# Kernel tuning notes

Measured on AMD Instinct MI355X. Metric: run time of the kernel, lower is better.

Reference implementation:

```python
import jax, jax.numpy as jnp
import numpy as np

K_MASK = -2.3819763e+38

B, T, D = 2, 2048, 2048
N_HEADS, N_KV, HEAD_DIM = 16, 8, 128
SCALAR = 0.08838834764831845  # head_dim ** -0.5
ROPE_BASE = 10000


def rms_norm(x, scale):
    # fp32 mean-of-squares, rsqrt, bf16 round-trip, then scale (as in QwemmaRMSNorm)
    x32 = x.astype(jnp.float32)
    var = jnp.mean(jnp.square(x32), axis=-1, keepdims=True)
    rescaled = (x32 * jax.lax.rsqrt(var + 1e-06)).astype(jnp.bfloat16)
    return rescaled * scale


def apply_rope(inputs, positions, base_frequency):
    head_dim = inputs.shape[-1]
    fraction = 2 * jnp.arange(0, head_dim // 2) / head_dim
    timescale = base_frequency ** fraction
    sinusoid = positions[..., jnp.newaxis] / timescale[jnp.newaxis, jnp.newaxis, :]
    sinusoid = sinusoid[..., jnp.newaxis, :]  # [B,T,1,H/2]
    sin = jnp.sin(sinusoid).astype(inputs.dtype)
    cos = jnp.cos(sinusoid).astype(inputs.dtype)
    first, second = jnp.split(inputs, 2, axis=-1)
    out = jnp.concatenate([first * cos - second * sin,
                           second * cos + first * sin], axis=-1)
    return out.astype(inputs.dtype)


def setup_inputs() -> dict:
    key = jax.random.key(0)
    ks = jax.random.split(key, 7)
    x = jax.random.normal(ks[0], (B, T, D), dtype=jnp.float32)
    segment_pos = jnp.broadcast_to(jnp.arange(T, dtype=jnp.int32)[None, :], (B, T))
    attn_mask = jnp.broadcast_to(jnp.tril(jnp.ones((T, T), dtype=bool))[None], (B, T, T))
    q_w = jax.random.normal(ks[1], (N_HEADS, D, HEAD_DIM), dtype=jnp.float32) * 0.02
    kv_w = jax.random.normal(ks[2], (2, N_KV, D, HEAD_DIM), dtype=jnp.float32) * 0.02
    o_w = jax.random.normal(ks[3], (N_HEADS, HEAD_DIM, D), dtype=jnp.float32) * 0.02
    q_scale = 1.0 + 0.1 * jax.random.normal(ks[4], (HEAD_DIM,), dtype=jnp.float32)
    k_scale = 1.0 + 0.1 * jax.random.normal(ks[5], (HEAD_DIM,), dtype=jnp.float32)
    return {"x": x, "segment_pos": segment_pos, "attn_mask": attn_mask,
            "q_w": q_w, "kv_w": kv_w, "o_w": o_w,
            "q_scale": q_scale, "k_scale": k_scale}


def reference(x, segment_pos, attn_mask, q_w, kv_w, o_w, q_scale, k_scale):
    # projections
    q = jnp.einsum('BTD,NDH->BTNH', x, q_w)
    k, v = jnp.einsum('BSD,CKDH->CBSKH', x, kv_w)
    # QK RMSNorm + RoPE
    q = apply_rope(rms_norm(q, q_scale), segment_pos, ROPE_BASE)
    k = apply_rope(rms_norm(k, k_scale), segment_pos, ROPE_BASE)
    # GQA: [B,T,N,H] -> [B,T,K,G,H]
    b, t, n, h = q.shape
    g = n // N_KV
    q = q.reshape((b, t, N_KV, g, h))
    logits = jnp.einsum('BTKGH,BSKH->BTKGS', q, k)
    logits = (logits.astype(jnp.float32) * SCALAR).astype(jnp.bfloat16)
    s = logits.shape[-1]
    logits = logits.reshape((b, t, n, s))
    padded = jnp.where(jnp.expand_dims(attn_mask, -2), logits, K_MASK)
    probs = jax.nn.softmax(padded.astype(jnp.float32), axis=-1).astype(k.dtype)
    probs = probs.reshape((b, t, N_KV, g, s))
    encoded = jnp.einsum('BTKGS,BSKH->BTKGH', probs, v)
    encoded = encoded.reshape((b, t, n, h))
    return jnp.einsum('BTNH,NHD->BTD', encoded, o_w)


if __name__ == '__main__':
    out = reference(**setup_inputs())
    print(out.shape, out.dtype)
```

## Files before the change

kernel.cpp:

```cpp
#include <hip/hip_runtime.h>

typedef unsigned short u16;
typedef __attribute__((ext_vector_type(4))) float f32x4;
typedef __attribute__((ext_vector_type(8))) short s16x8;

#define SCALAR_F 0.08838834764831845f
#define KMASKF (-1e30f)

__device__ __forceinline__ u16 f2b(float f){
  unsigned u = __float_as_uint(f);
  unsigned r = u + 0x7FFFu + ((u>>16)&1u);
  return (u16)(r>>16);
}
__device__ __forceinline__ float b2f(u16 h){ return __uint_as_float(((unsigned)h)<<16); }

__device__ __forceinline__ f32x4 mfma16(s16x8 a, s16x8 b, f32x4 c){
  return __builtin_amdgcn_mfma_f32_16x16x32_bf16(a, b, c, 0, 0, 0);
}

__device__ __forceinline__ void glds16(const u16* g, u16* l){
  __builtin_amdgcn_global_load_lds((const __attribute__((address_space(1))) unsigned*)g,
                                   (__attribute__((address_space(3))) unsigned*)l, 16, 0, 0);
}

#define PHASE_BAR() asm volatile("s_barrier" ::: "memory")
#define LGKM0()     do { asm volatile("s_waitcnt lgkmcnt(0)" ::: "memory"); __builtin_amdgcn_sched_barrier(0); } while(0)

__global__ __launch_bounds__(256) void cvt_f32_bf16(const float* __restrict__ in, u16* __restrict__ out){
  int i = blockIdx.x*256 + threadIdx.x;
  const float4* p = (const float4*)in;
  float4 a = p[2*i], b = p[2*i+1];
  s16x8 r;
  r[0]=(short)f2b(a.x); r[1]=(short)f2b(a.y); r[2]=(short)f2b(a.z); r[3]=(short)f2b(a.w);
  r[4]=(short)f2b(b.x); r[5]=(short)f2b(b.y); r[6]=(short)f2b(b.z); r[7]=(short)f2b(b.w);
  *(s16x8*)(out + (size_t)i*8) = r;
}

__global__ __launch_bounds__(256) void build_wqkvt(const float* __restrict__ qw, const float* __restrict__ kvw,
                                                   u16* __restrict__ out){
  __shared__ float t[64][65];
  int head = blockIdx.z;
  int d0 = blockIdx.y*64, h0 = blockIdx.x*64;
  const float* src; int colbase;
  if (head < 16){ src = qw + (size_t)head*2048*128; colbase = head*128; }
  else if (head < 24){ int k = head-16; src = kvw + (size_t)k*2048*128; colbase = 2048 + k*128; }
  else { int k = head-24; src = kvw + (size_t)(8+k)*2048*128; colbase = 3072 + k*128; }
  int tid = threadIdx.x;
  #pragma unroll
  for (int p=0;p<16;p++){ int e = p*256+tid; int r = e>>6, c = e&63;
    t[r][c] = src[(size_t)(d0+r)*128 + h0 + c]; }
  __syncthreads();
  #pragma unroll
  for (int p=0;p<16;p++){ int e = p*256+tid; int c = e>>6, r = e&63;
    out[(size_t)(colbase + h0 + c)*2048 + d0 + r] = f2b(t[r][c]); }
}

__global__ __launch_bounds__(256) void tr2048(const float* __restrict__ src, u16* __restrict__ out){
  __shared__ float t[64][65];
  int r0 = blockIdx.y*64, c0 = blockIdx.x*64;
  int tid = threadIdx.x;
  #pragma unroll
  for (int p=0;p<16;p++){ int e = p*256+tid; int r = e>>6, c = e&63;
    t[r][c] = src[(size_t)(r0+r)*2048 + c0 + c]; }
  __syncthreads();
  #pragma unroll
  for (int p=0;p<16;p++){ int e = p*256+tid; int c = e>>6, r = e&63;
    out[(size_t)(c0+c)*2048 + r0 + r] = f2b(t[r][c]); }
}

__global__ __launch_bounds__(256) void rope_table(float* __restrict__ table){
  int tid = blockIdx.x*256 + threadIdx.x;
  int pos = tid>>6, i = tid&63;
  float ts = powf(10000.f, (float)i * (1.f/64.f));
  float ang = (float)pos / ts;
  ((float2*)table)[tid] = make_float2(sinf(ang), cosf(ang));
}

__global__ __launch_bounds__(512,2) void gemm256(const u16* __restrict__ A, const u16* __restrict__ Bt,
                                                 u16* __restrict__ C, int K, int ldc){
  __shared__ u16 Als[2][2][128*64];
  __shared__ u16 Bls[2][2][128*64];
  const int tid = threadIdx.x;
  const int wid = tid>>6, l = tid&63;
  const int wr = wid>>2, wc = wid&3;
  const int l15 = l&15, lg = l>>4;
  const int wg = blockIdx.x;
  const int swz = (wg&7)*32 + (wg>>3);
  const size_t m0 = (size_t)(swz>>4)*256, n0 = (size_t)(swz&15)*256;

  const f32x4 z4 = {0.f,0.f,0.f,0.f};
  f32x4 acc[8][4];
  #pragma unroll
  for (int mi=0;mi<8;mi++)
    #pragma unroll
    for (int ni=0;ni<4;ni++) acc[mi][ni] = z4;

  auto stageA = [&](int k0, int bi, int h){
    #pragma unroll
    for (int c=0;c<2;c++){
      int g = c*512 + tid;
      int row = g>>3, pg = g&7;
      glds16(A + (m0 + h*128 + row)*K + k0 + ((pg ^ (row&7))<<3), &Als[bi][h][0] + g*8);
    }
  };
  auto stageB = [&](int k0, int bi, int h){
    #pragma unroll
    for (int c=0;c<2;c++){
      int g = c*512 + tid;
      int row = g>>3, pg = g&7;
      glds16(Bt + (n0 + h*128 + row)*K + k0 + ((pg ^ (row&7))<<3), &Bls[bi][h][0] + g*8);
    }
  };

  s16x8 af[8][2], bf[4][2];

  const int NT = K>>6;
  stageA(0,0,0); stageA(0,0,1); stageB(0,0,0); stageB(0,0,1);
  stageA(64,1,0); stageA(64,1,1);
  asm volatile("s_waitcnt vmcnt(4)" ::: "memory");
  PHASE_BAR();

  for (int t=0; t<NT; ++t){
    const int bi = t&1;
    const char* Ab = (const char*)&Als[bi][wr][0];
    const char* Bb = (const char*)&Bls[bi][wc>>1][0];
    const int brl = (wc&1)*64;
    const int kn1 = (t+1)<<6, kn2 = (t+2)<<6;

    #pragma unroll
    for (int mi=0;mi<4;mi++){
      int r = mi*16 + l15;
      #pragma unroll
      for (int kk=0;kk<2;kk++)
        af[mi][kk] = *(const s16x8*)(Ab + r*128 + (((kk*4+lg) ^ (r&7))<<4));
    }
    #pragma unroll
    for (int ni=0;ni<2;ni++){
      int r = brl + ni*16 + l15;
      #pragma unroll
      for (int kk=0;kk<2;kk++)
        bf[ni][kk] = *(const s16x8*)(Bb + r*128 + (((kk*4+lg) ^ (r&7))<<4));
    }
    if (t+1 < NT) stageB(kn1, bi^1, 0);
    PHASE_BAR(); LGKM0();
    __builtin_amdgcn_s_setprio(1);
    #pragma unroll
    for (int mi=0;mi<4;mi++)
      #pragma unroll
      for (int ni=0;ni<2;ni++)
        #pragma unroll
        for (int kk=0;kk<2;kk++)
          acc[mi][ni] = mfma16(af[mi][kk], bf[ni][kk], acc[mi][ni]);
    __builtin_amdgcn_s_setprio(0);
    PHASE_BAR();

    #pragma unroll
    for (int ni=2;ni<4;ni++){
      int r = brl + ni*16 + l15;
      #pragma unroll
      for (int kk=0;kk<2;kk++)
        bf[ni][kk] = *(const s16x8*)(Bb + r*128 + (((kk*4+lg) ^ (r&7))<<4));
    }
    if (t+1 < NT) stageB(kn1, bi^1, 1);
    PHASE_BAR(); LGKM0();
    __builtin_amdgcn_s_setprio(1);
    #pragma unroll
    for (int mi=0;mi<4;mi++)
      #pragma unroll
      for (int ni=2;ni<4;ni++)
        #pragma unroll
        for (int kk=0;kk<2;kk++)
          acc[mi][ni] = mfma16(af[mi][kk], bf[ni][kk], acc[mi][ni]);
    __builtin_amdgcn_s_setprio(0);
    PHASE_BAR();

    #pragma unroll
    for (int mi=4;mi<8;mi++){
      int r = mi*16 + l15;
      #pragma unroll
      for (int kk=0;kk<2;kk++)
        af[mi][kk] = *(const s16x8*)(Ab + r*128 + (((kk*4+lg) ^ (r&7))<<4));
    }
    PHASE_BAR(); LGKM0();
    __builtin_amdgcn_s_setprio(1);
    #pragma unroll
    for (int mi=4;mi<8;mi++)
      #pragma unroll
      for (int ni=2;ni<4;ni++)
        #pragma unroll
        for (int kk=0;kk<2;kk++)
          acc[mi][ni] = mfma16(af[mi][kk], bf[ni][kk], acc[mi][ni]);
    __builtin_amdgcn_s_setprio(0);
    PHASE_BAR();

    if (t+2 < NT){ stageA(kn2, bi, 0); stageA(kn2, bi, 1); }
    __builtin_amdgcn_s_setprio(1);
    #pragma unroll
    for (int mi=4;mi<8;mi++)
      #pragma unroll
      for (int ni=0;ni<2;ni++)
        #pragma unroll
        for (int kk=0;kk<2;kk++)
          acc[mi][ni] = mfma16(af[mi][kk], bf[ni][kk], acc[mi][ni]);
    __builtin_amdgcn_s_setprio(0);
    if (t < NT-2)      { asm volatile("s_waitcnt vmcnt(4)" ::: "memory"); }
    else if (t == NT-2){ asm volatile("s_waitcnt vmcnt(0)" ::: "memory"); }
    PHASE_BAR();
  }

  #pragma unroll
  for (int mi=0;mi<8;mi++)
    #pragma unroll
    for (int ni=0;ni<4;ni++)
      #pragma unroll
      for (int r=0;r<4;r++){
        size_t row = m0 + wr*128 + mi*16 + lg*4 + r;
        size_t col = n0 + wc*64 + ni*16 + l15;
        C[row*ldc + col] = f2b(acc[mi][ni][r]);
      }
}

__global__ __launch_bounds__(512,1) void gemm_o(const u16* __restrict__ A, const u16* __restrict__ Bt,
                                                float* __restrict__ C, int K, int ldc){
  __shared__ u16 Als[2][2][128*64];
  __shared__ u16 Bls[2][128*64];
  const int tid = threadIdx.x;
  const int wid = tid>>6, l = tid&63;
  const int wr = wid>>1, wc = wid&1;
  const int l15 = l&15, lg = l>>4;
  const int wg = blockIdx.x;
  const int swz = (wg&7)*32 + (wg>>3);
  const size_t m0 = (size_t)(swz>>4)*256, n0 = (size_t)(swz&15)*128;

  const f32x4 z4 = {0.f,0.f,0.f,0.f};
  f32x4 acc[4][4];
  #pragma unroll
  for (int mi=0;mi<4;mi++)
    #pragma unroll
    for (int ni=0;ni<4;ni++) acc[mi][ni] = z4;

  auto stageA = [&](int k0, int bi, int h){
    #pragma unroll
    for (int c=0;c<2;c++){
      int g = c*512 + tid;
      int row = g>>3, pg = g&7;
      glds16(A + (m0 + h*128 + row)*K + k0 + ((pg ^ (row&7))<<3), &Als[bi][h][0] + g*8);
    }
  };
  auto stageB = [&](int k0, int bi){
    #pragma unroll
    for (int c=0;c<2;c++){
      int g = c*512 + tid;
      int row = g>>3, pg = g&7;
      glds16(Bt + (n0 + row)*K + k0 + ((pg ^ (row&7))<<3), &Bls[bi][0] + g*8);
    }
  };

  s16x8 af[4][2], bf[4][2];

  const int NT = K>>6;
  stageA(0,0,0); stageA(0,0,1); stageB(0,0);
  stageA(64,1,0); stageA(64,1,1);
  asm volatile("s_waitcnt vmcnt(4)" ::: "memory");
  PHASE_BAR();

  for (int t=0; t<NT; ++t){
    const int bi = t&1;
    const char* Ab = (const char*)&Als[bi][wr>>1][0];
    const char* Bb = (const char*)&Bls[bi][0];
    const int arl = (wr&1)*64;
    const int brl = wc*64;
    const int kn1 = (t+1)<<6, kn2 = (t+2)<<6;

    #pragma unroll
    for (int mi=0;mi<2;mi++){
      int r = arl + mi*16 + l15;
      #pragma unroll
      for (int kk=0;kk<2;kk++)
        af[mi][kk] = *(const s16x8*)(Ab + r*128 + (((kk*4+lg) ^ (r&7))<<4));
    }
    #pragma unroll
    for (int ni=0;ni<2;ni++){
      int r = brl + ni*16 + l15;
      #pragma unroll
      for (int kk=0;kk<2;kk++)
        bf[ni][kk] = *(const s16x8*)(Bb + r*128 + (((kk*4+lg) ^ (r&7))<<4));
    }
    if (t+1 < NT) stageB(kn1, bi^1);
    PHASE_BAR(); LGKM0();
    __builtin_amdgcn_s_setprio(1);
    #pragma unroll
    for (int mi=0;mi<2;mi++)
      #pragma unroll
      for (int ni=0;ni<2;ni++)
        #pragma unroll
        for (int kk=0;kk<2;kk++)
          acc[mi][ni] = mfma16(af[mi][kk], bf[ni][kk], acc[mi][ni]);
    __builtin_amdgcn_s_setprio(0);
    PHASE_BAR();

    #pragma unroll
    for (int mi=2;mi<4;mi++){
      int r = arl + mi*16 + l15;
      #pragma unroll
      for (int kk=0;kk<2;kk++)
        af[mi][kk] = *(const s16x8*)(Ab + r*128 + (((kk*4+lg) ^ (r&7))<<4));
    }
    #pragma unroll
    for (int ni=2;ni<4;ni++){
      int r = brl + ni*16 + l15;
      #pragma unroll
      for (int kk=0;kk<2;kk++)
        bf[ni][kk] = *(const s16x8*)(Bb + r*128 + (((kk*4+lg) ^ (r&7))<<4));
    }
    PHASE_BAR(); LGKM0();
    __builtin_amdgcn_s_setprio(1);
    #pragma unroll
    for (int mi=0;mi<2;mi++)
      #pragma unroll
      for (int ni=2;ni<4;ni++)
        #pragma unroll
        for (int kk=0;kk<2;kk++)
          acc[mi][ni] = mfma16(af[mi][kk], bf[ni][kk], acc[mi][ni]);
    __builtin_amdgcn_s_setprio(0);
    PHASE_BAR();

    if (t+2 < NT){ stageA(kn2, bi, 0); stageA(kn2, bi, 1); }
    __builtin_amdgcn_s_setprio(1);
    #pragma unroll
    for (int mi=2;mi<4;mi++)
      #pragma unroll
      for (int ni=0;ni<4;ni++)
        #pragma unroll
        for (int kk=0;kk<2;kk++)
          acc[mi][ni] = mfma16(af[mi][kk], bf[ni][kk], acc[mi][ni]);
    __builtin_amdgcn_s_setprio(0);
    if (t < NT-2)      { asm volatile("s_waitcnt vmcnt(4)" ::: "memory"); }
    else if (t == NT-2){ asm volatile("s_waitcnt vmcnt(0)" ::: "memory"); }
    PHASE_BAR();
  }

  #pragma unroll
  for (int mi=0;mi<4;mi++)
    #pragma unroll
    for (int ni=0;ni<4;ni++)
      #pragma unroll
      for (int r=0;r<4;r++){
        size_t row = m0 + wr*64 + mi*16 + lg*4 + r;
        size_t col = n0 + wc*64 + ni*16 + l15;
        C[row*ldc + col] = acc[mi][ni][r];
      }
}

__global__ __launch_bounds__(256) void norm_rope(const u16* __restrict__ qkv, const float* __restrict__ table,
                                                 const float* __restrict__ scale, const int* __restrict__ segpos,
                                                 u16* __restrict__ dst, int nhl2, int colbase, float mult){
  int w = threadIdx.x>>6, l = threadIdx.x&63;
  int rid = blockIdx.x*4 + w;
  int bt = rid >> nhl2;
  int n  = rid & ((1<<nhl2)-1);
  int b = bt >> 11, t = bt & 2047;
  const u16* src = qkv + (size_t)bt*4096 + colbase + n*128;
  float x1 = b2f(src[l]), x2 = b2f(src[64+l]);
  float ss = x1*x1 + x2*x2;
  #pragma unroll
  for (int off=32; off; off>>=1) ss += __shfl_xor(ss, off);
  float rs = rsqrtf(ss*(1.f/128.f) + 1e-6f);
  float v1 = x1*rs*scale[l], v2 = x2*rs*scale[64+l];
  int pos = segpos[bt];
  float2 sc = ((const float2*)table)[pos*64 + l];
  float o1 = (v1*sc.y - v2*sc.x)*mult;
  float o2 = (v2*sc.y + v1*sc.x)*mult;
  u16* d = dst + (((size_t)((b<<nhl2) + n))*2048 + t)*128;
  d[l] = f2b(o1); d[64+l] = f2b(o2);
}

__global__ __launch_bounds__(256) void vtr(const u16* __restrict__ qkv, u16* __restrict__ vt){
  __shared__ float t[64][65];
  int bk = blockIdx.z;
  int t0 = blockIdx.y*64, d0 = blockIdx.x*64;
  int b = bk>>3, kv = bk&7;
  int tid = threadIdx.x;
  #pragma unroll
  for (int p=0;p<16;p++){ int e = p*256+tid; int r = e>>6, c = e&63;
    t[r][c] = b2f(qkv[(size_t)(b*2048 + t0 + r)*4096 + 3072 + kv*128 + d0 + c]); }
  __syncthreads();
  #pragma unroll
  for (int p=0;p<16;p++){ int e = p*256+tid; int c = e>>6, r = e&63;
    vt[((size_t)bk*128 + d0 + c)*2048 + t0 + r] = f2b(t[r][c]); }
}

__global__ __launch_bounds__(256,2) void attn_kern(const u16* __restrict__ qn, const u16* __restrict__ kn,
                                                   const u16* __restrict__ vt, u16* __restrict__ enc){
  __shared__ u16 Ks[2][64*128];
  __shared__ u16 Vs[2][64*128];
  __shared__ u16 Ps[4*16*64];
  const int idx = blockIdx.x;
  const int pp = idx>>5;
  const int hb = idx & 31;
  const int hn = hb & 15, b = hb >> 4;
  const int kv = hn>>1;
  const int tid = threadIdx.x, w = tid>>6, l = tid&63;
  const int l15 = l&15, lg = l>>4;
  const u16* qh = qn + ((size_t)(b*16+hn))*2048*128;
  const u16* kh = kn + ((size_t)(b*8+kv))*2048*128;
  const u16* vh = vt + ((size_t)(b*8+kv))*128*2048;
  const int qbA = pp, qbB = 31-pp;

  int qr0 = qbA*64 + w*16;
  s16x8 qf[4];
  #pragma unroll
  for (int kb=0;kb<4;kb++)
    qf[kb] = *(const s16x8*)(qh + (size_t)(qr0 + l15)*128 + kb*32 + lg*8);

  const f32x4 z4 = {0.f,0.f,0.f,0.f};
  f32x4 o[8];
  #pragma unroll
  for (int dn=0;dn<8;dn++) o[dn] = z4;
  float mrow[4], lp[4];
  #pragma unroll
  for (int r=0;r<4;r++){ mrow[r] = KMASKF; lp[r] = 0.f; }

  const char* KsB0 = (const char*)&Ks[0][0];
  const char* VsB0 = (const char*)&Vs[0][0];
  char* PsB = (char*)Ps + w*2048;

  auto stage = [&](int s0, int bi){
    #pragma unroll
    for (int i=0;i<4;i++){
      int slot = (w*4+i)*64 + l;
      { int row = slot>>4, g = slot&15, gl = g ^ (row&7);
        glds16(kh + (size_t)(s0+row)*128 + gl*8, &Ks[bi][0] + slot*8); }
      { int row = slot>>3, g = slot&7, gl = g ^ (row&7);
        glds16(vh + (size_t)row*2048 + s0 + gl*8, &Vs[bi][0] + slot*8); }
    }
  };

  auto epilogue = [&](int qr){
    #pragma unroll
    for (int r=0;r<4;r++){
      float s = lp[r];
      s += __shfl_xor(s,1); s += __shfl_xor(s,2); s += __shfl_xor(s,4); s += __shfl_xor(s,8);
      lp[r] = 1.f/s;
    }
    #pragma unroll
    for (int dn=0;dn<8;dn++)
      #pragma unroll
      for (int r=0;r<4;r++){
        size_t row = (size_t)b*2048 + qr + lg*4 + r;
        size_t col = hn*128 + dn*16 + l15;
        enc[row*2048 + col] = f2b(o[dn][r]*lp[r]);
      }
  };

  stage(0, 0);
  __syncthreads();

  int cur = 0;
  for (int it=0; it<=32; ++it){
    if (it < 32){
      int s0n = (it+1 <= pp) ? (it+1)*64 : (it-pp)*64;
      stage(s0n, cur^1);
    }
    const int s0 = (it <= pp) ? it*64 : (it-pp-1)*64;
    const char* KsB = KsB0 + cur*16384;
    const char* VsB = VsB0 + cur*16384;

    f32x4 sa[4];
    #pragma unroll
    for (int nc=0;nc<4;nc++) sa[nc] = z4;
    #pragma unroll
    for (int kb=0;kb<4;kb++){
      s16x8 kf[4];
      #pragma unroll
      for (int nc=0;nc<4;nc++){
        int srow = nc*16 + l15;
        int cb = (kb*64 + lg*16) ^ ((srow&7)<<4);
        kf[nc] = *(const s16x8*)(KsB + srow*256 + cb);
      }
      __builtin_amdgcn_s_setprio(1);
      #pragma unroll
      for (int nc=0;nc<4;nc++)
        sa[nc] = mfma16(qf[kb], kf[nc], sa[nc]);
      __builtin_amdgcn_s_setprio(0);
    }
    if (it == pp || it == 32){
      #pragma unroll
      for (int nc=0;nc<4;nc++)
        #pragma unroll
        for (int r=0;r<4;r++){
          int row = qr0 + lg*4 + r;
          int col = s0 + nc*16 + l15;
          if (col > row) sa[nc][r] = KMASKF;
        }
    }
    #pragma unroll
    for (int r=0;r<4;r++){
      float pm = fmaxf(fmaxf(sa[0][r], sa[1][r]), fmaxf(sa[2][r], sa[3][r]));
      pm = fmaxf(pm, __shfl_xor(pm,1));
      pm = fmaxf(pm, __shfl_xor(pm,2));
      pm = fmaxf(pm, __shfl_xor(pm,4));
      pm = fmaxf(pm, __shfl_xor(pm,8));
      float mo = mrow[r];
      float mn = mo;
      if (!__all(pm <= mo + 8.f)){
        mn = fmaxf(mo, pm);
        float sc = __expf(mo - mn);
        mrow[r] = mn;
        lp[r] *= sc;
        #pragma unroll
        for (int dn=0;dn<8;dn++) o[dn][r] *= sc;
      }
      int rowp = lg*4 + r;
      float ls = 0.f;
      #pragma unroll
      for (int nc=0;nc<4;nc++){
        float p = __expf(sa[nc][r] - mn);
        ls += p;
        int cb = ((nc*16 + l15)*2) ^ ((rowp&7)<<4);
        *(u16*)(PsB + rowp*128 + cb) = f2b(p);
      }
      lp[r] += ls;
    }
    asm volatile("" ::: "memory");
    #pragma unroll
    for (int kb=0;kb<2;kb++){
      int rowp = l15;
      int cbp = (kb*64 + lg*16) ^ ((rowp&7)<<4);
      s16x8 pf = *(const s16x8*)(PsB + rowp*128 + cbp);
      #pragma unroll
      for (int dn=0;dn<8;dn++){
        int vrow = dn*16 + l15;
        int cb = (kb*64 + lg*16) ^ ((vrow&7)<<4);
        s16x8 vf = *(const s16x8*)(VsB + vrow*128 + cb);
        __builtin_amdgcn_s_setprio(1);
        o[dn] = mfma16(pf, vf, o[dn]);
        __builtin_amdgcn_s_setprio(0);
      }
    }
    if (it == pp){
      epilogue(qr0);
      qr0 = qbB*64 + w*16;
      #pragma unroll
      for (int kb=0;kb<4;kb++)
        qf[kb] = *(const s16x8*)(qh + (size_t)(qr0 + l15)*128 + kb*32 + lg*8);
      #pragma unroll
      for (int dn=0;dn<8;dn++) o[dn] = z4;
      #pragma unroll
      for (int r=0;r<4;r++){ mrow[r] = KMASKF; lp[r] = 0.f; }
    }
    __syncthreads();
    cur ^= 1;
  }
  epilogue(qr0);
}

extern "C" void kernel_launch(void* const* d_in, const int* in_sizes, int n_in,
                              void* d_out, int out_size, void* d_ws, size_t ws_size,
                              hipStream_t stream){
  const float* x      = (const float*)d_in[0];
  const int*   segpos = (const int*)d_in[1];
  const float* qw     = (const float*)d_in[3];
  const float* kvw    = (const float*)d_in[4];
  const float* ow     = (const float*)d_in[5];
  const float* qs     = (const float*)d_in[6];
  const float* ks     = (const float*)d_in[7];
  float* out = (float*)d_out;

  char* ws = (char*)d_ws;
  size_t off = 0;
  auto alloc = [&](size_t bytes)->void*{ void* p = ws + off; off += (bytes + 255) & ~(size_t)255; return p; };
  u16*   xb    = (u16*)alloc((size_t)4096*2048*2);
  u16*   wqkvt = (u16*)alloc((size_t)4096*2048*2);
  u16*   wot   = (u16*)alloc((size_t)2048*2048*2);
  u16*   qkv   = (u16*)alloc((size_t)4096*4096*2);
  u16*   qn    = (u16*)alloc((size_t)2*16*2048*128*2);
  u16*   kn    = (u16*)alloc((size_t)2*8*2048*128*2);
  u16*   vt    = (u16*)alloc((size_t)2*8*128*2048*2);
  u16*   enc   = (u16*)alloc((size_t)4096*2048*2);
  float* table = (float*)alloc((size_t)2048*64*2*4);

  cvt_f32_bf16<<<4096,256,0,stream>>>(x, xb);
  build_wqkvt<<<dim3(2,32,32),256,0,stream>>>(qw, kvw, wqkvt);
  tr2048<<<dim3(32,32),256,0,stream>>>(ow, wot);
  rope_table<<<512,256,0,stream>>>(table);
  gemm256<<<256,512,0,stream>>>(xb, wqkvt, qkv, 2048, 4096);
  norm_rope<<<16384,256,0,stream>>>(qkv, table, qs, segpos, qn, 4, 0,    SCALAR_F);
  norm_rope<<<8192, 256,0,stream>>>(qkv, table, ks, segpos, kn, 3, 2048, 1.0f);
  vtr<<<dim3(2,32,16),256,0,stream>>>(qkv, vt);
  attn_kern<<<512,256,0,stream>>>(qn, kn, vt, enc);
  gemm_o<<<256,512,0,stream>>>(enc, wot, out, 2048, 2048);
}
```

Baseline: 366.2 us.

## Merge prep and norm kernels, drop lazy rescale and setprio in attention

Merges the x conversion and rope-table kernels into one launch, the two weight-transpose kernels into another, and the Q and K norm_rope launches into one grid, cutting the launch count from ten to seven. Each merged kernel picks its work by block index. In the attention inner loop, the conditional lazy rescale (skip unless the max grows by more than 8) becomes an unconditional rescale of the accumulators on every tile. The s_setprio hints around the MFMA calls are also removed. The unconditional rescale adds per-tile multiplies but removes a wave-wide vote and branch.

Result: faster. 354.0 us (-3.3%).

```diff
diff --git a/kernel.cpp b/kernel.cpp
--- a/kernel.cpp
+++ b/kernel.cpp
@@ -26,54 +26,57 @@
 #define PHASE_BAR() asm volatile("s_barrier" ::: "memory")
 #define LGKM0()     do { asm volatile("s_waitcnt lgkmcnt(0)" ::: "memory"); __builtin_amdgcn_sched_barrier(0); } while(0)
 
-__global__ __launch_bounds__(256) void cvt_f32_bf16(const float* __restrict__ in, u16* __restrict__ out){
-  int i = blockIdx.x*256 + threadIdx.x;
-  const float4* p = (const float4*)in;
-  float4 a = p[2*i], b = p[2*i+1];
-  s16x8 r;
-  r[0]=(short)f2b(a.x); r[1]=(short)f2b(a.y); r[2]=(short)f2b(a.z); r[3]=(short)f2b(a.w);
-  r[4]=(short)f2b(b.x); r[5]=(short)f2b(b.y); r[6]=(short)f2b(b.z); r[7]=(short)f2b(b.w);
-  *(s16x8*)(out + (size_t)i*8) = r;
-}
-
-__global__ __launch_bounds__(256) void build_wqkvt(const float* __restrict__ qw, const float* __restrict__ kvw,
-                                                   u16* __restrict__ out){
+__global__ __launch_bounds__(256) void prep_misc(const float* __restrict__ in, u16* __restrict__ out,
+                                                 float* __restrict__ table){
+  int bid = blockIdx.x;
+  if (bid < 4096){
+    int i = bid*256 + threadIdx.x;
+    const float4* p = (const float4*)in;
+    float4 a = p[2*i], b = p[2*i+1];
+    s16x8 r;
+    r[0]=(short)f2b(a.x); r[1]=(short)f2b(a.y); r[2]=(short)f2b(a.z); r[3]=(short)f2b(a.w);
+    r[4]=(short)f2b(b.x); r[5]=(short)f2b(b.y); r[6]=(short)f2b(b.z); r[7]=(short)f2b(b.w);
+    *(s16x8*)(out + (size_t)i*8) = r;
+  } else {
+    int tid = (bid-4096)*256 + threadIdx.x;
+    int pos = tid>>6, i = tid&63;
+    float ts = powf(10000.f, (float)i * (1.f/64.f));
+    float ang = (float)pos / ts;
+    ((float2*)table)[tid] = make_float2(sinf(ang), cosf(ang));
+  }
+}
+
+__global__ __launch_bounds__(256) void prep_w(const float* __restrict__ qw, const float* __restrict__ kvw,
+                                              const float* __restrict__ ow,
+                                              u16* __restrict__ wqkvt, u16* __restrict__ wot){
   __shared__ float t[64][65];
-  int head = blockIdx.z;
-  int d0 = blockIdx.y*64, h0 = blockIdx.x*64;
-  const float* src; int colbase;
-  if (head < 16){ src = qw + (size_t)head*2048*128; colbase = head*128; }
-  else if (head < 24){ int k = head-16; src = kvw + (size_t)k*2048*128; colbase = 2048 + k*128; }
-  else { int k = head-24; src = kvw + (size_t)(8+k)*2048*128; colbase = 3072 + k*128; }
+  int idx = blockIdx.x;
   int tid = threadIdx.x;
-  #pragma unroll
-  for (int p=0;p<16;p++){ int e = p*256+tid; int r = e>>6, c = e&63;
-    t[r][c] = src[(size_t)(d0+r)*128 + h0 + c]; }
-  __syncthreads();
-  #pragma unroll
-  for (int p=0;p<16;p++){ int e = p*256+tid; int c = e>>6, r = e&63;
-    out[(size_t)(colbase + h0 + c)*2048 + d0 + r] = f2b(t[r][c]); }
-}
-
-__global__ __launch_bounds__(256) void tr2048(const float* __restrict__ src, u16* __restrict__ out){
-  __shared__ float t[64][65];
-  int r0 = blockIdx.y*64, c0 = blockIdx.x*64;
-  int tid = threadIdx.x;
-  #pragma unroll
-  for (int p=0;p<16;p++){ int e = p*256+tid; int r = e>>6, c = e&63;
-    t[r][c] = src[(size_t)(r0+r)*2048 + c0 + c]; }
-  __syncthreads();
-  #pragma unroll
-  for (int p=0;p<16;p++){ int e = p*256+tid; int c = e>>6, r = e&63;
-    out[(size_t)(c0+c)*2048 + r0 + r] = f2b(t[r][c]); }
-}
-
-__global__ __launch_bounds__(256) void rope_table(float* __restrict__ table){
-  int tid = blockIdx.x*256 + threadIdx.x;
-  int pos = tid>>6, i = tid&63;
-  float ts = powf(10000.f, (float)i * (1.f/64.f));
-  float ang = (float)pos / ts;
-  ((float2*)table)[tid] = make_float2(sinf(ang), cosf(ang));
+  if (idx < 2048){
+    int head = idx>>6;
+    int d0 = ((idx>>1)&31)*64, h0 = (idx&1)*64;
+    const float* src; int colbase;
+    if (head < 16){ src = qw + (size_t)head*2048*128; colbase = head*128; }
+    else if (head < 24){ int k = head-16; src = kvw + (size_t)k*2048*128; colbase = 2048 + k*128; }
+    else { int k = head-24; src = kvw + (size_t)(8+k)*2048*128; colbase = 3072 + k*128; }
+    #pragma unroll
+    for (int p=0;p<16;p++){ int e = p*256+tid; int r = e>>6, c = e&63;
+      t[r][c] = src[(size_t)(d0+r)*128 + h0 + c]; }
+    __syncthreads();
+    #pragma unroll
+    for (int p=0;p<16;p++){ int e = p*256+tid; int c = e>>6, r = e&63;
+      wqkvt[(size_t)(colbase + h0 + c)*2048 + d0 + r] = f2b(t[r][c]); }
+  } else {
+    int j = idx - 2048;
+    int r0 = (j>>5)*64, c0 = (j&31)*64;
+    #pragma unroll
+    for (int p=0;p<16;p++){ int e = p*256+tid; int r = e>>6, c = e&63;
+      t[r][c] = ow[(size_t)(r0+r)*2048 + c0 + c]; }
+    __syncthreads();
+    #pragma unroll
+    for (int p=0;p<16;p++){ int e = p*256+tid; int c = e>>6, r = e&63;
+      wot[(size_t)(c0+c)*2048 + r0 + r] = f2b(t[r][c]); }
+  }
 }
 
 __global__ __launch_bounds__(512,2) void gemm256(const u16* __restrict__ A, const u16* __restrict__ Bt,
@@ -353,10 +356,15 @@
 }
 
 __global__ __launch_bounds__(256) void norm_rope(const u16* __restrict__ qkv, const float* __restrict__ table,
-                                                 const float* __restrict__ scale, const int* __restrict__ segpos,
-                                                 u16* __restrict__ dst, int nhl2, int colbase, float mult){
+                                                 const float* __restrict__ qscale, const float* __restrict__ kscale,
+                                                 const int* __restrict__ segpos,
+                                                 u16* __restrict__ qn, u16* __restrict__ kn){
   int w = threadIdx.x>>6, l = threadIdx.x&63;
-  int rid = blockIdx.x*4 + w;
+  int idx = blockIdx.x;
+  int nhl2, colbase; float mult; const float* scale; u16* dst;
+  int rid;
+  if (idx < 16384){ nhl2 = 4; colbase = 0;    mult = SCALAR_F; scale = qscale; dst = qn; rid = idx*4 + w; }
+  else            { nhl2 = 3; colbase = 2048; mult = 1.0f;     scale = kscale; dst = kn; rid = (idx-16384)*4 + w; }
   int bt = rid >> nhl2;
   int n  = rid & ((1<<nhl2)-1);
   int b = bt >> 11, t = bt & 2047;
@@ -478,11 +486,9 @@
         int cb = (kb*64 + lg*16) ^ ((srow&7)<<4);
         kf[nc] = *(const s16x8*)(KsB + srow*256 + cb);
       }
-      __builtin_amdgcn_s_setprio(1);
       #pragma unroll
       for (int nc=0;nc<4;nc++)
         sa[nc] = mfma16(qf[kb], kf[nc], sa[nc]);
-      __builtin_amdgcn_s_setprio(0);
     }
     if (it == pp || it == 32){
       #pragma unroll
@@ -502,15 +508,9 @@
       pm = fmaxf(pm, __shfl_xor(pm,4));
       pm = fmaxf(pm, __shfl_xor(pm,8));
       float mo = mrow[r];
-      float mn = mo;
-      if (!__all(pm <= mo + 8.f)){
-        mn = fmaxf(mo, pm);
-        float sc = __expf(mo - mn);
-        mrow[r] = mn;
-        lp[r] *= sc;
-        #pragma unroll
-        for (int dn=0;dn<8;dn++) o[dn][r] *= sc;
-      }
+      float mn = fmaxf(mo, pm);
+      float sc = __expf(mo - mn);
+      mrow[r] = mn;
       int rowp = lg*4 + r;
       float ls = 0.f;
       #pragma unroll
@@ -520,7 +520,9 @@
         int cb = ((nc*16 + l15)*2) ^ ((rowp&7)<<4);
         *(u16*)(PsB + rowp*128 + cb) = f2b(p);
       }
-      lp[r] += ls;
+      lp[r] = lp[r]*sc + ls;
+      #pragma unroll
+      for (int dn=0;dn<8;dn++) o[dn][r] *= sc;
     }
     asm volatile("" ::: "memory");
     #pragma unroll
@@ -533,9 +535,7 @@
         int vrow = dn*16 + l15;
         int cb = (kb*64 + lg*16) ^ ((vrow&7)<<4);
         s16x8 vf = *(const s16x8*)(VsB + vrow*128 + cb);
-        __builtin_amdgcn_s_setprio(1);
         o[dn] = mfma16(pf, vf, o[dn]);
-        __builtin_amdgcn_s_setprio(0);
       }
     }
     if (it == pp){
@@ -580,13 +580,10 @@
   u16*   enc   = (u16*)alloc((size_t)4096*2048*2);
   float* table = (float*)alloc((size_t)2048*64*2*4);
 
-  cvt_f32_bf16<<<4096,256,0,stream>>>(x, xb);
-  build_wqkvt<<<dim3(2,32,32),256,0,stream>>>(qw, kvw, wqkvt);
-  tr2048<<<dim3(32,32),256,0,stream>>>(ow, wot);
-  rope_table<<<512,256,0,stream>>>(table);
+  prep_misc<<<4608,256,0,stream>>>(x, xb, table);
+  prep_w<<<3072,256,0,stream>>>(qw, kvw, ow, wqkvt, wot);
   gemm256<<<256,512,0,stream>>>(xb, wqkvt, qkv, 2048, 4096);
-  norm_rope<<<16384,256,0,stream>>>(qkv, table, qs, segpos, qn, 4, 0,    SCALAR_F);
-  norm_rope<<<8192, 256,0,stream>>>(qkv, table, ks, segpos, kn, 3, 2048, 1.0f);
+  norm_rope<<<24576,256,0,stream>>>(qkv, table, qs, ks, segpos, qn, kn);
   vtr<<<dim3(2,32,16),256,0,stream>>>(qkv, vt);
   attn_kern<<<512,256,0,stream>>>(qn, kn, vt, enc);
   gemm_o<<<256,512,0,stream>>>(enc, wot, out, 2048, 2048);
```
